# Performance work log

Hardware: AMD Instinct MI355X
Metric: run time of the kernel (lower is better)

The kernel has to match this reference:

```python
import jax, jax.numpy as jnp
import numpy as np

GROUPS = 32
EPS = 1e-5


def group_norm(x, gamma, beta):
    # x: [b, h, w, c] NHWC; normalize over (h, w, c/GROUPS) within each group
    b, h, w, c = x.shape
    xg = x.reshape(b, h, w, GROUPS, c // GROUPS)
    mean = jnp.mean(xg, axis=(1, 2, 4), keepdims=True)
    var = jnp.var(xg, axis=(1, 2, 4), keepdims=True)
    xg = (xg - mean) * jax.lax.rsqrt(var + EPS)
    return xg.reshape(b, h, w, c) * gamma + beta


def setup_inputs() -> dict:
    key = jax.random.key(0)
    ks = jax.random.split(key, 6)
    c = 512
    s = 1.0 / np.sqrt(c)  # fan-in scaled init for conv weights
    return {
        "x": jax.random.normal(ks[0], (2, 64, 64, c), dtype=jnp.float32),
        "gamma": jnp.ones((c,), jnp.float32),
        "beta": jnp.zeros((c,), jnp.float32),
        "wq": jax.random.normal(ks[1], (c, c), jnp.float32) * s,
        "bq": jnp.zeros((c,), jnp.float32),
        "wk": jax.random.normal(ks[2], (c, c), jnp.float32) * s,
        "bk": jnp.zeros((c,), jnp.float32),
        "wv": jax.random.normal(ks[3], (c, c), jnp.float32) * s,
        "bv": jnp.zeros((c,), jnp.float32),
        "wo": jax.random.normal(ks[4], (c, c), jnp.float32) * s,
        "bo": jnp.zeros((c,), jnp.float32),
    }


def reference(x, gamma, beta, wq, bq, wk, bk, wv, bv, wo, bo):
    b, h, w, c = x.shape
    n = h * w
    hn = group_norm(x, gamma, beta)
    hn = hn.reshape(b, n, c)  # flatten spatial -> tokens
    # 1x1 convs == pointwise linear
    q = hn @ wq + bq  # [b, n, c]
    k = hn @ wk + bk
    v = hn @ wv + bv
    scores = jnp.einsum("bic,bjc->bij", q, k) * (c ** -0.5)  # [b, n, n]
    attn = jax.nn.softmax(scores, axis=-1)
    out = jnp.einsum("bij,bjc->bic", attn, v)  # [b, n, c]
    out = out @ wo + bo
    return x + out.reshape(b, h, w, c)
```

## Files before the change

kernel.cpp:

```cpp
#include <hip/hip_runtime.h>
#include <hip/hip_fp8.h>
#include <stdint.h>


typedef unsigned short u16;
typedef unsigned char u8;
typedef short s16x8 __attribute__((ext_vector_type(8)));
typedef float f32x4 __attribute__((ext_vector_type(4)));
typedef int i32x8 __attribute__((ext_vector_type(8)));
typedef float f32x16 __attribute__((ext_vector_type(16)));

#define NTOK 4096
#define CH   512

__device__ inline u16 f2bf(float f) {
  union { float f; uint32_t u; } v; v.f = f;
  uint32_t r = v.u + 0x7FFFu + ((v.u >> 16) & 1u);
  return (u16)(r >> 16);
}
__device__ inline float bf2f(u16 b) {
  union { uint32_t u; float f; } v; v.u = (uint32_t)b << 16; return v.f;
}
__device__ inline f32x4 mfma16(s16x8 a, s16x8 b, f32x4 c) {
  return __builtin_amdgcn_mfma_f32_16x16x32_bf16(a, b, c, 0, 0, 0);
}
__device__ inline f32x16 mfma_mx8(i32x8 a, i32x8 b, f32x16 c) {
  return __builtin_amdgcn_mfma_scale_f32_32x32x64_f8f6f4(
      a, b, c, 0 , 0 ,
      0, 0x7F7F7F7F, 0, 0x7F7F7F7F);
}
__device__ inline uint32_t pk_fp8x4(float e0, float e1, float e2, float e3) {
#if __has_builtin(__builtin_amdgcn_cvt_pk_fp8_f32)
  int v = __builtin_amdgcn_cvt_pk_fp8_f32(e0, e1, 0, false);
  v = __builtin_amdgcn_cvt_pk_fp8_f32(e2, e3, v, true);
  return (uint32_t)v;
#else
  __hip_fp8_e4m3 a(e0), b(e1), c(e2), d(e3);
  return (uint32_t)*(u8*)&a | ((uint32_t)*(u8*)&b << 8) |
         ((uint32_t)*(u8*)&c << 16) | ((uint32_t)*(u8*)&d << 24);
#endif
}
__device__ inline u8 f2fp8(float x) {
#if __has_builtin(__builtin_amdgcn_cvt_pk_fp8_f32)
  int v = __builtin_amdgcn_cvt_pk_fp8_f32(x, x, 0, false);
  return (u8)(v & 0xFF);
#else
  __hip_fp8_e4m3 h(x); return *(u8*)&h;
#endif
}
__device__ inline void gload_lds16(const void* g, void* l) {
  __builtin_amdgcn_global_load_lds(
      (const __attribute__((address_space(1))) unsigned*)g,
      (__attribute__((address_space(3))) unsigned*)l, 16, 0, 0);
}
__device__ inline uint4 addbf8(uint4 a, uint4 b) {
  union { uint4 v; u16 h[8]; } A, B, O; A.v = a; B.v = b;
#pragma unroll
  for (int j = 0; j < 8; j++) O.h[j] = f2bf(bf2f(A.h[j]) + bf2f(B.h[j]));
  return O.v;
}

__global__ __launch_bounds__(256) void gn_stats_kernel(
    const float* __restrict__ x, float* __restrict__ part) {
  int c = blockIdx.x, b = blockIdx.y;
  int t = threadIdx.x, g = t & 31;
  const float* xb = x + (size_t)b * NTOK * CH + (size_t)c * 64 * CH + g * 16;
  float s = 0.f, q = 0.f;
  for (int p = 0; p < 8; p++) {
    const float* ptr = xb + ((size_t)p * 8 + (t >> 5)) * CH;
#pragma unroll
    for (int j = 0; j < 4; j++) {
      float4 v = *(const float4*)(ptr + j * 4);
      s += v.x + v.y + v.z + v.w;
      q += v.x * v.x + v.y * v.y + v.z * v.z + v.w * v.w;
    }
  }
  __shared__ float ls[32][8], lq[32][8];
  ls[g][t >> 5] = s; lq[g][t >> 5] = q;
  __syncthreads();
  if (t < 32) {
    float S = 0.f, Q = 0.f;
#pragma unroll
    for (int j = 0; j < 8; j++) { S += ls[t][j]; Q += lq[t][j]; }
    float2 o; o.x = S; o.y = Q;
    *(float2*)&part[(((size_t)b * 64 + c) * 32 + t) * 2] = o;
  }
}

__global__ __launch_bounds__(256) void gn_apply_kernel(
    const float* __restrict__ x, const float* __restrict__ part,
    const float* __restrict__ gamma, const float* __restrict__ beta,
    u16* __restrict__ hn) {
  int blk = blockIdx.x, b = blk >> 9, t = threadIdx.x;
  __shared__ float msh[32], rsh[32];
  if (t < 64) {
    int g = t >> 1, half = t & 1;
    float S = 0.f, Q = 0.f;
    for (int c = half * 32; c < half * 32 + 32; c++) {
      float2 p = *(const float2*)&part[(((size_t)b * 64 + c) * 32 + g) * 2];
      S += p.x; Q += p.y;
    }
    S += __shfl_xor(S, 1, 64);
    Q += __shfl_xor(Q, 1, 64);
    if (half == 0) {
      float mean = S * (1.f / 65536.f);
      float var = Q * (1.f / 65536.f) - mean * mean;
      msh[g] = mean; rsh[g] = rsqrtf(var + 1e-5f);
    }
  }
  __syncthreads();
  size_t base = (size_t)b * NTOK * CH + (size_t)(blk & 511) * 4096 + t * 16;
  int ch0 = (t * 16) & 511;
  float mean = msh[t & 31], rstd = rsh[t & 31];
  const float* xp = x + base;
  union { u16 h[16]; uint4 v[2]; } o;
#pragma unroll
  for (int j = 0; j < 4; j++) {
    float4 xv = *(const float4*)(xp + j * 4);
    float4 gv = *(const float4*)(gamma + ch0 + j * 4);
    float4 bv = *(const float4*)(beta + ch0 + j * 4);
    o.h[j * 4 + 0] = f2bf((xv.x - mean) * rstd * gv.x + bv.x);
    o.h[j * 4 + 1] = f2bf((xv.y - mean) * rstd * gv.y + bv.y);
    o.h[j * 4 + 2] = f2bf((xv.z - mean) * rstd * gv.z + bv.z);
    o.h[j * 4 + 3] = f2bf((xv.w - mean) * rstd * gv.w + bv.w);
  }
  *(uint4*)(hn + base) = o.v[0];
  *(uint4*)(hn + base + 8) = o.v[1];
}

__global__ __launch_bounds__(256) void wprep_kernel(
    const float* w0, const float* w1, const float* w2, const float* w3,
    u16* t0, u16* t1, u16* t2, u16* t3) {
  int z = blockIdx.z;
  const float* w = z == 0 ? w0 : z == 1 ? w1 : z == 2 ? w2 : w3;
  u16* wt = z == 0 ? t0 : z == 1 ? t1 : z == 2 ? t2 : t3;
  __shared__ float tile[32][33];
  int k0 = blockIdx.x * 32, n0 = blockIdx.y * 32;
  int tx = threadIdx.x & 31, ty = threadIdx.x >> 5;
  for (int r = 0; r < 4; r++)
    tile[ty * 4 + r][tx] = w[(size_t)(k0 + ty * 4 + r) * CH + n0 + tx];
  __syncthreads();
  for (int r = 0; r < 4; r++)
    wt[(size_t)(n0 + ty * 4 + r) * CH + k0 + tx] = f2bf(tile[tx][ty * 4 + r]);
}

__global__ __launch_bounds__(256, 2) void qkv_gemm_kernel(
    const u16* __restrict__ A, const u16* __restrict__ Wcat,
    const float* __restrict__ bq, const float* __restrict__ bk,
    const float* __restrict__ bvv, u8* __restrict__ qf8, u8* __restrict__ kf8,
    u8* __restrict__ vtf8) {
  __shared__ __align__(16) u8 pool[65536];
  int m0 = blockIdx.x * 128, n0 = blockIdx.y * 128;
  int t = threadIdx.x, lane = t & 63, wave = t >> 6;
  int wx = wave & 1, wy = wave >> 1;
  int lane4 = lane >> 4;
  f32x4 acc[4][4] = {};
  const u16 *Asrc[4], *Bsrc[4];
  int dsto[4];
#pragma unroll
  for (int j = 0; j < 4; j++) {
    int u = t + j * 256, row = u >> 3, ch = (u & 7) ^ (row & 7);
    Asrc[j] = A + (size_t)(m0 + row) * CH + ch * 8;
    Bsrc[j] = Wcat + (size_t)(n0 + row) * CH + ch * 8;
    dsto[j] = u * 16;
  }
#pragma unroll
  for (int j = 0; j < 4; j++) {
    gload_lds16(Asrc[j], pool + dsto[j]);
    gload_lds16(Bsrc[j], pool + 32768 + dsto[j]);
  }
  __syncthreads();
  for (int kt = 0; kt < 8; kt++) {
    int co = (kt & 1) * 16384;
    const u16* Ac = (const u16*)(pool + co);
    const u16* Bc = (const u16*)(pool + 32768 + co);
    if (kt < 7) {
      int no = ((kt & 1) ^ 1) * 16384;
#pragma unroll
      for (int j = 0; j < 4; j++) {
        Asrc[j] += 64; Bsrc[j] += 64;
        gload_lds16(Asrc[j], pool + no + dsto[j]);
        gload_lds16(Bsrc[j], pool + 32768 + no + dsto[j]);
      }
    }
    __builtin_amdgcn_s_setprio(1);
#pragma unroll
    for (int ks = 0; ks < 2; ks++) {
      int kc = ks * 4 + lane4;
      s16x8 af[4], bf[4];
#pragma unroll
      for (int i = 0; i < 4; i++) {
        int ra = wx * 64 + i * 16 + (lane & 15);
        af[i] = *(const s16x8*)&Ac[ra * 64 + ((kc ^ (ra & 7)) << 3)];
        int rb = wy * 64 + i * 16 + (lane & 15);
        bf[i] = *(const s16x8*)&Bc[rb * 64 + ((kc ^ (rb & 7)) << 3)];
      }
#pragma unroll
      for (int mi = 0; mi < 4; mi++)
#pragma unroll
        for (int ni = 0; ni < 4; ni++)
          acc[mi][ni] = mfma16(af[mi], bf[ni], acc[mi][ni]);
    }
    __builtin_amdgcn_s_setprio(0);
    __syncthreads();
  }
  int proj = n0 >> 9;
  int r0l = wx * 64 + lane4 * 4;
  if (proj <= 1) {
    u8* O = proj == 0 ? qf8 : kf8;
    const float* bias = proj == 0 ? bq : bk;
#pragma unroll
    for (int mi = 0; mi < 4; mi++)
#pragma unroll
      for (int ni = 0; ni < 4; ni++) {
        int colp = (n0 & 511) + wy * 64 + ni * 16 + (lane & 15);
        float bv = bias[colp];
#pragma unroll
        for (int r = 0; r < 4; r++)
          O[(size_t)(m0 + r0l + mi * 16 + r) * CH + colp] =
              f2fp8(acc[mi][ni][r] + bv);
      }
  } else {
#pragma unroll
    for (int mi = 0; mi < 4; mi++)
#pragma unroll
      for (int ni = 0; ni < 4; ni++) {
        int colp = (n0 & 511) + wy * 64 + ni * 16 + (lane & 15);
        float bv = bvv[colp];
        int row = m0 + r0l + mi * 16;
        int bb = row >> 12, nn = row & 4095;
        uint32_t p = pk_fp8x4(acc[mi][ni][0] + bv, acc[mi][ni][1] + bv,
                              acc[mi][ni][2] + bv, acc[mi][ni][3] + bv);
        *(uint32_t*)&vtf8[((size_t)bb * CH + colp) * NTOK + nn] = p;
      }
  }
}

__global__ __launch_bounds__(256) void gemm_out_kernel(
    const u16* __restrict__ A, const u16* __restrict__ A2,
    const u16* __restrict__ Wt, const float* __restrict__ bias,
    float* __restrict__ out, const float* __restrict__ xres) {
  __shared__ __align__(16) u16 As[128 * 40];
  __shared__ __align__(16) u16 Bs[64 * 40];
  int m0 = blockIdx.x * 128, n0 = blockIdx.y * 64;
  int t = threadIdx.x, lane = t & 63, wave = t >> 6;
  int wm = wave >> 1, wn = wave & 1;
  f32x4 acc[4][2] = {};
  int arow = t >> 2, ac = t & 3;
  size_t aoff = (size_t)(m0 + arow) * CH + ac * 8;
  const u16* Bg = Wt + (size_t)(n0 + arow) * CH + ac * 8;
  uint4 a0 = addbf8(*(const uint4*)(A + aoff), *(const uint4*)(A2 + aoff));
  uint4 a1 = addbf8(*(const uint4*)(A + aoff + 64 * CH),
                    *(const uint4*)(A2 + aoff + 64 * CH));
  uint4 b0 = *(const uint4*)Bg;
  for (int kt = 0; kt < 16; kt++) {
    __syncthreads();
    *(uint4*)&As[(size_t)arow * 40 + ac * 8] = a0;
    *(uint4*)&As[(size_t)(arow + 64) * 40 + ac * 8] = a1;
    *(uint4*)&Bs[(size_t)arow * 40 + ac * 8] = b0;
    if (kt < 15) {
      aoff += 32; Bg += 32;
      a0 = addbf8(*(const uint4*)(A + aoff), *(const uint4*)(A2 + aoff));
      a1 = addbf8(*(const uint4*)(A + aoff + 64 * CH),
                  *(const uint4*)(A2 + aoff + 64 * CH));
      b0 = *(const uint4*)Bg;
    }
    __syncthreads();
    s16x8 af[4], bfr[2];
#pragma unroll
    for (int i = 0; i < 4; i++)
      af[i] = *(const s16x8*)&As[(wm * 64 + i * 16 + (lane & 15)) * 40 + (lane >> 4) * 8];
#pragma unroll
    for (int j = 0; j < 2; j++)
      bfr[j] = *(const s16x8*)&Bs[(wn * 32 + j * 16 + (lane & 15)) * 40 + (lane >> 4) * 8];
    __builtin_amdgcn_s_setprio(1);
#pragma unroll
    for (int mi = 0; mi < 4; mi++)
#pragma unroll
      for (int ni = 0; ni < 2; ni++)
        acc[mi][ni] = mfma16(af[mi], bfr[ni], acc[mi][ni]);
    __builtin_amdgcn_s_setprio(0);
  }
  int r0l = wm * 64 + ((lane >> 4) * 4);
  int c0l = wn * 32 + (lane & 15);
#pragma unroll
  for (int mi = 0; mi < 4; mi++)
#pragma unroll
    for (int ni = 0; ni < 2; ni++) {
      int col = n0 + c0l + ni * 16;
      float bv = bias[col];
#pragma unroll
      for (int r = 0; r < 4; r++) {
        size_t idx = (size_t)(m0 + r0l + mi * 16 + r) * CH + col;
        out[idx] = xres[idx] + acc[mi][ni][r] + bv;
      }
    }
}

__global__ __launch_bounds__(256, 2) void s_gemm_kernel(
    const u8* __restrict__ qf8, const u8* __restrict__ kf8,
    u8* __restrict__ S, float* __restrict__ lpart) {
  const float QS = 0.044194173824159216f;
  __shared__ __align__(16) u8 pool[65536];
  int bz = blockIdx.z;
  const u8* qb = qf8 + (size_t)bz * NTOK * CH;
  const u8* kb = kf8 + (size_t)bz * NTOK * CH;
  u8* Sg = S + (size_t)bz * NTOK * NTOK;
  float* lp = lpart + (size_t)bz * 64 * NTOK;
  int m0 = blockIdx.x * 128, n0 = blockIdx.y * 128;
  int t = threadIdx.x, lane = t & 63, wave = t >> 6;
  int wmx = wave & 1, wy = wave >> 1;
  int lh = lane >> 5;
  f32x16 acc[2][2] = {};
  const u8 *Asrc[4], *Bsrc[4];
  int dsto[4];
#pragma unroll
  for (int j = 0; j < 4; j++) {
    int u = t + j * 256, row = u >> 3, ch = (u & 7) ^ (row & 7);
    Asrc[j] = kb + (size_t)(n0 + row) * CH + ch * 16;
    Bsrc[j] = qb + (size_t)(m0 + row) * CH + ch * 16;
    dsto[j] = u * 16;
  }
#pragma unroll
  for (int j = 0; j < 4; j++) {
    gload_lds16(Asrc[j], pool + dsto[j]);
    gload_lds16(Bsrc[j], pool + 32768 + dsto[j]);
  }
  __syncthreads();
  for (int kt = 0; kt < 4; kt++) {
    int co = (kt & 1) * 16384;
    const u8* Ac = pool + co;
    const u8* Bc = pool + 32768 + co;
    if (kt < 3) {
      int no = ((kt & 1) ^ 1) * 16384;
#pragma unroll
      for (int j = 0; j < 4; j++) {
        Asrc[j] += 128; Bsrc[j] += 128;
        gload_lds16(Asrc[j], pool + no + dsto[j]);
        gload_lds16(Bsrc[j], pool + 32768 + no + dsto[j]);
      }
    }
    __builtin_amdgcn_s_setprio(1);
#pragma unroll
    for (int kh = 0; kh < 2; kh++) {
      int cb = kh * 4 + lh * 2;
      union { i32x8 v; uint4 qq[2]; } bu[2];
#pragma unroll
      for (int bj = 0; bj < 2; bj++) {
        int rb = wmx * 64 + bj * 32 + (lane & 31);
        const u8* bp = &Bc[rb * 128];
        bu[bj].qq[0] = *(const uint4*)&bp[(cb ^ (rb & 7)) << 4];
        bu[bj].qq[1] = *(const uint4*)&bp[((cb + 1) ^ (rb & 7)) << 4];
      }
#pragma unroll
      for (int ai = 0; ai < 2; ai++) {
        int ra = wy * 64 + ai * 32 + (lane & 31);
        union { i32x8 v; uint4 qq[2]; } au;
        const u8* ap = &Ac[ra * 128];
        au.qq[0] = *(const uint4*)&ap[(cb ^ (ra & 7)) << 4];
        au.qq[1] = *(const uint4*)&ap[((cb + 1) ^ (ra & 7)) << 4];
#pragma unroll
        for (int bj = 0; bj < 2; bj++)
          acc[ai][bj] = mfma_mx8(au.v, bu[bj].v, acc[ai][bj]);
      }
    }
    __builtin_amdgcn_s_setprio(0);
    __syncthreads();
  }
  uint32_t* Stile = (uint32_t*)pool;
  float psum[2] = {};
#pragma unroll
  for (int ai = 0; ai < 2; ai++) {
#pragma unroll
    for (int bj = 0; bj < 2; bj++) {
      int ml = wmx * 64 + bj * 32 + (lane & 31);
#pragma unroll
      for (int qd = 0; qd < 4; qd++) {
        float e0 = __expf(acc[ai][bj][qd * 4 + 0] * QS);
        float e1 = __expf(acc[ai][bj][qd * 4 + 1] * QS);
        float e2 = __expf(acc[ai][bj][qd * 4 + 2] * QS);
        float e3 = __expf(acc[ai][bj][qd * 4 + 3] * QS);
        psum[bj] += e0 + e1 + e2 + e3;
        int nw = wy * 16 + ai * 8 + qd * 2 + lh;
        Stile[ml * 32 + (nw ^ ((ml & 7) << 2))] = pk_fp8x4(e0, e1, e2, e3);
      }
    }
  }
#pragma unroll
  for (int bj = 0; bj < 2; bj++) {
    float v = psum[bj];
    v += __shfl_xor(v, 32, 64);
    if (lane < 32) {
      int m = m0 + wmx * 64 + bj * 32 + lane;
      lp[(size_t)((n0 >> 6) + wy) * NTOK + m] = v;
    }
  }
  __syncthreads();
#pragma unroll
  for (int p = 0; p < 4; p++) {
    int row = (t >> 3) + p * 32;
    int g = t & 7;
    int w0 = (g * 4) ^ ((row & 7) << 2);
    uint4 v;
    v.x = Stile[row * 32 + w0 + 0];
    v.y = Stile[row * 32 + w0 + 1];
    v.z = Stile[row * 32 + w0 + 2];
    v.w = Stile[row * 32 + w0 + 3];
    *(uint4*)&Sg[(size_t)(m0 + row) * NTOK + n0 + g * 16] = v;
  }
}

__global__ __launch_bounds__(256, 2) void pv_gemm_kernel(
    const u8* __restrict__ S, const u8* __restrict__ vtf8,
    const float* __restrict__ lpart, u16* __restrict__ part0,
    u16* __restrict__ part1) {
  __shared__ __align__(16) u8 Asw[2][16384];
  __shared__ __align__(16) u8 Bsw[2][16384];
  __shared__ float linv_s[128];
  int flat = blockIdx.x + 32 * blockIdx.y + 128 * blockIdx.z;
  int xcd = flat & 7, u = flat >> 3;
  int m_t = xcd * 4 + (u & 3);
  int n_i = (u >> 2) & 3;
  int spb = u >> 4, sp = spb & 1, b = spb >> 1;
  int m0 = m_t * 128, n0 = n_i * 128, kbase = sp * 2048;
  const u8* Sb = S + (size_t)b * NTOK * NTOK;
  const u8* vb = vtf8 + (size_t)b * CH * NTOK;
  const float* lp = lpart + (size_t)b * 64 * NTOK;
  int t = threadIdx.x, lane = t & 63, wave = t >> 6;
  int wm = wave >> 1, wn = wave & 1;
  int lh = lane >> 5;
  f32x16 acc[2][2] = {};
  const u8 *Asrc[4], *Bsrc[4];
  int uoff[4];
#pragma unroll
  for (int j = 0; j < 4; j++) {
    int uu = t + j * 256, row = uu >> 3, ch = (uu & 7) ^ (row & 7);
    Asrc[j] = Sb + (size_t)(m0 + row) * NTOK + kbase + ch * 16;
    Bsrc[j] = vb + (size_t)(n0 + row) * NTOK + kbase + ch * 16;
    uoff[j] = uu * 16;
  }
#pragma unroll
  for (int j = 0; j < 4; j++) {
    gload_lds16(Asrc[j], &Asw[0][uoff[j]]);
    gload_lds16(Bsrc[j], &Bsw[0][uoff[j]]);
  }
  __syncthreads();
  int cur = 0;
  for (int kt = 0; kt < 16; kt++) {
    if (kt < 15) {
#pragma unroll
      for (int j = 0; j < 4; j++) {
        Asrc[j] += 128; Bsrc[j] += 128;
        gload_lds16(Asrc[j], &Asw[cur ^ 1][uoff[j]]);
        gload_lds16(Bsrc[j], &Bsw[cur ^ 1][uoff[j]]);
      }
    }
    __builtin_amdgcn_s_setprio(1);
#pragma unroll
    for (int kh = 0; kh < 2; kh++) {
      int cb = kh * 4 + lh * 2;
      union { i32x8 v; uint4 qq[2]; } bu[2];
#pragma unroll
      for (int ni = 0; ni < 2; ni++) {
        int rb = wn * 64 + ni * 32 + (lane & 31);
        const u8* bp = &Bsw[cur][rb * 128];
        bu[ni].qq[0] = *(const uint4*)&bp[(cb ^ (rb & 7)) << 4];
        bu[ni].qq[1] = *(const uint4*)&bp[((cb + 1) ^ (rb & 7)) << 4];
      }
#pragma unroll
      for (int mi = 0; mi < 2; mi++) {
        int ra = wm * 64 + mi * 32 + (lane & 31);
        union { i32x8 v; uint4 qq[2]; } au;
        const u8* ap = &Asw[cur][ra * 128];
        au.qq[0] = *(const uint4*)&ap[(cb ^ (ra & 7)) << 4];
        au.qq[1] = *(const uint4*)&ap[((cb + 1) ^ (ra & 7)) << 4];
#pragma unroll
        for (int ni = 0; ni < 2; ni++)
          acc[mi][ni] = mfma_mx8(au.v, bu[ni].v, acc[mi][ni]);
      }
    }
    __builtin_amdgcn_s_setprio(0);
    __syncthreads();
    cur ^= 1;
  }
  if (t < 128) {
    float s = 0.f;
#pragma unroll 8
    for (int c = 0; c < 64; c++) s += lp[(size_t)c * NTOK + m0 + t];
    linv_s[t] = 1.f / s;
  }
  __syncthreads();
  u16* Od = (sp ? part1 : part0) + (size_t)b * NTOK * CH;
#pragma unroll
  for (int mi = 0; mi < 2; mi++)
#pragma unroll
    for (int ni = 0; ni < 2; ni++)
#pragma unroll
      for (int reg = 0; reg < 16; reg++) {
        int crow = (reg & 3) + 8 * (reg >> 2) + 4 * lh;
        int gr = wm * 64 + mi * 32 + crow;
        Od[(size_t)(m0 + gr) * CH + n0 + wn * 64 + ni * 32 + (lane & 31)] =
            f2bf(acc[mi][ni][reg] * linv_s[gr]);
      }
}

extern "C" void kernel_launch(void* const* d_in, const int* in_sizes, int n_in,
                              void* d_out, int out_size, void* d_ws, size_t ws_size,
                              hipStream_t stream) {
  const float* x     = (const float*)d_in[0];
  const float* gamma = (const float*)d_in[1];
  const float* beta  = (const float*)d_in[2];
  const float* wq    = (const float*)d_in[3];
  const float* bq    = (const float*)d_in[4];
  const float* wk    = (const float*)d_in[5];
  const float* bk    = (const float*)d_in[6];
  const float* wv    = (const float*)d_in[7];
  const float* bv    = (const float*)d_in[8];
  const float* wo    = (const float*)d_in[9];
  const float* bo    = (const float*)d_in[10];

  char* ws = (char*)d_ws;
  u16* hn   = (u16*)(ws + 0);
  u16* q    = (u16*)(ws + 8388608);
  u8*  vtf8 = (u8*)(ws + 25165824);
  u16* wqt  = (u16*)(ws + 33554432);
  u16* wkt  = (u16*)(ws + 34078720);
  u16* wvt  = (u16*)(ws + 34603008);
  u16* wot  = (u16*)(ws + 35127296);
  u8*  S    = (u8*)(ws + 35651584);
  float* lpart = (float*)(ws + 71303168);
  u8*  qf8  = (u8*)(ws + 75497472);
  u8*  kf8  = (u8*)(ws + 79691776);

  float* gnpart = (float*)q;

  gn_stats_kernel<<<dim3(64, 2), 256, 0, stream>>>(x, gnpart);
  wprep_kernel<<<dim3(16, 16, 4), 256, 0, stream>>>(wq, wk, wv, wo, wqt, wkt, wvt, wot);
  gn_apply_kernel<<<1024, 256, 0, stream>>>(x, gnpart, gamma, beta, hn);
  qkv_gemm_kernel<<<dim3(64, 12), 256, 0, stream>>>(hn, wqt, bq, bk, bv, qf8, kf8, vtf8);
  s_gemm_kernel<<<dim3(32, 32, 2), 256, 0, stream>>>(qf8, kf8, S, lpart);
  pv_gemm_kernel<<<dim3(32, 4, 4), 256, 0, stream>>>(S, vtf8, lpart, hn, q);
  gemm_out_kernel<<<dim3(64, 8), 256, 0, stream>>>(hn, q, wot, bo, (float*)d_out, x);
}
```

Measured before the change: 115.2 us.

## Keep two LDS tiles in flight with counted vmcnt waits in attention GEMMs

Both the QK^T score kernel and the PV kernel now issue loads for two k-tiles up front. Each iteration waits only until the current tile has arrived, using s_waitcnt vmcnt(8) and raw s_barrier calls. The load into the freed buffer is issued right after the compute barrier instead of at the top of the loop. This is meant to hide more global-to-LDS latency and to avoid the full vmcnt(0) drain that __syncthreads forces. It depends on the exact count of outstanding loads per thread and on sched_barrier ordering, which makes the code fragile if the load count changes.

```diff
diff --git a/kernel.cpp b/kernel.cpp
--- a/kernel.cpp
+++ b/kernel.cpp
@@ -58,6 +58,19 @@
 #pragma unroll
   for (int j = 0; j < 8; j++) O.h[j] = f2bf(bf2f(A.h[j]) + bf2f(B.h[j]));
   return O.v;
+}
+__device__ inline void wait_vm8() {
+  asm volatile("s_waitcnt vmcnt(8)" ::: "memory");
+  __builtin_amdgcn_sched_barrier(0);
+}
+__device__ inline void wait_vm0() {
+  asm volatile("s_waitcnt vmcnt(0)" ::: "memory");
+  __builtin_amdgcn_sched_barrier(0);
+}
+__device__ inline void barrier_raw() {
+  __builtin_amdgcn_sched_barrier(0);
+  __builtin_amdgcn_s_barrier();
+  __builtin_amdgcn_sched_barrier(0);
 }
 
 __global__ __launch_bounds__(256) void gn_stats_kernel(
@@ -326,20 +339,20 @@
     gload_lds16(Asrc[j], pool + dsto[j]);
     gload_lds16(Bsrc[j], pool + 32768 + dsto[j]);
   }
-  __syncthreads();
+#pragma unroll
+  for (int j = 0; j < 4; j++) {
+    Asrc[j] += 128; Bsrc[j] += 128;
+    gload_lds16(Asrc[j], pool + 16384 + dsto[j]);
+    gload_lds16(Bsrc[j], pool + 32768 + 16384 + dsto[j]);
+  }
+  __builtin_amdgcn_sched_barrier(0);
+#pragma unroll
   for (int kt = 0; kt < 4; kt++) {
+    if (kt < 3) wait_vm8(); else wait_vm0();
+    barrier_raw();
     int co = (kt & 1) * 16384;
     const u8* Ac = pool + co;
     const u8* Bc = pool + 32768 + co;
-    if (kt < 3) {
-      int no = ((kt & 1) ^ 1) * 16384;
-#pragma unroll
-      for (int j = 0; j < 4; j++) {
-        Asrc[j] += 128; Bsrc[j] += 128;
-        gload_lds16(Asrc[j], pool + no + dsto[j]);
-        gload_lds16(Bsrc[j], pool + 32768 + no + dsto[j]);
-      }
-    }
     __builtin_amdgcn_s_setprio(1);
 #pragma unroll
     for (int kh = 0; kh < 2; kh++) {
@@ -365,7 +378,15 @@
       }
     }
     __builtin_amdgcn_s_setprio(0);
-    __syncthreads();
+    barrier_raw();
+    if (kt < 2) {
+#pragma unroll
+      for (int j = 0; j < 4; j++) {
+        Asrc[j] += 128; Bsrc[j] += 128;
+        gload_lds16(Asrc[j], pool + co + dsto[j]);
+        gload_lds16(Bsrc[j], pool + 32768 + co + dsto[j]);
+      }
+    }
   }
   uint32_t* Stile = (uint32_t*)pool;
   float psum[2] = {};
@@ -444,17 +465,17 @@
     gload_lds16(Asrc[j], &Asw[0][uoff[j]]);
     gload_lds16(Bsrc[j], &Bsw[0][uoff[j]]);
   }
-  __syncthreads();
-  int cur = 0;
+#pragma unroll
+  for (int j = 0; j < 4; j++) {
+    Asrc[j] += 128; Bsrc[j] += 128;
+    gload_lds16(Asrc[j], &Asw[1][uoff[j]]);
+    gload_lds16(Bsrc[j], &Bsw[1][uoff[j]]);
+  }
+  __builtin_amdgcn_sched_barrier(0);
   for (int kt = 0; kt < 16; kt++) {
-    if (kt < 15) {
-#pragma unroll
-      for (int j = 0; j < 4; j++) {
-        Asrc[j] += 128; Bsrc[j] += 128;
-        gload_lds16(Asrc[j], &Asw[cur ^ 1][uoff[j]]);
-        gload_lds16(Bsrc[j], &Bsw[cur ^ 1][uoff[j]]);
-      }
-    }
+    if (kt < 15) wait_vm8(); else wait_vm0();
+    barrier_raw();
+    int cur = kt & 1;
     __builtin_amdgcn_s_setprio(1);
 #pragma unroll
     for (int kh = 0; kh < 2; kh++) {
@@ -480,8 +501,15 @@
       }
     }
     __builtin_amdgcn_s_setprio(0);
-    __syncthreads();
-    cur ^= 1;
+    barrier_raw();
+    if (kt < 14) {
+#pragma unroll
+      for (int j = 0; j < 4; j++) {
+        Asrc[j] += 128; Bsrc[j] += 128;
+        gload_lds16(Asrc[j], &Asw[cur][uoff[j]]);
+        gload_lds16(Bsrc[j], &Bsw[cur][uoff[j]]);
+      }
+    }
   }
   if (t < 128) {
     float s = 0.f;
```

After: 114.6 us. About the same (-0.5%).
